# Optimization experiments

Hardware: AMD Instinct MI355X
Metric: run time of the kernel (lower is better)

Reference implementation:

```python
import jax, jax.numpy as jnp
import numpy as np

N, E = 50000, 800000
F_IN, HID, HEADS = 128, 32, 8
H1 = HID * HEADS            # 256: conv1 concat output, also conv2 in/out
NUM_WALKS, WALK_LEN = 512, 64
WINDOW, NEG_S = 5, 10
TEMP = 0.07
NEG_SLOPE = 0.2


def setup_inputs() -> dict:
    key = jax.random.key(0)
    ks = jax.random.split(key, 16)
    inp = {
        "x": jax.random.normal(ks[0], (N, F_IN), jnp.float32),
        "edge_index": jax.random.randint(ks[1], (2, E), 0, N),
        "walks": jax.random.randint(ks[2], (NUM_WALKS, WALK_LEN), 0, N),
        "neg_nodes": jax.random.randint(ks[3], (NUM_WALKS, WALK_LEN, NEG_S), 0, N),
        # conv1 params (GATConv: in=F_IN, out=HID, heads=HEADS, concat)
        "W1": jax.random.normal(ks[4], (F_IN, HEADS * HID), jnp.float32) / np.sqrt(F_IN),
        "a_src1": jax.random.normal(ks[5], (HEADS, HID), jnp.float32) / np.sqrt(HID),
        "a_dst1": jax.random.normal(ks[6], (HEADS, HID), jnp.float32) / np.sqrt(HID),
        "b1": jnp.zeros((HEADS * HID,), jnp.float32),
        # conv2 params (GATConv: in=H1, out=H1, heads=1)
        "W2": jax.random.normal(ks[7], (H1, H1), jnp.float32) / np.sqrt(H1),
        "a_src2": jax.random.normal(ks[8], (1, H1), jnp.float32) / np.sqrt(H1),
        "a_dst2": jax.random.normal(ks[9], (1, H1), jnp.float32) / np.sqrt(H1),
        "b2": jnp.zeros((H1,), jnp.float32),
    }
    return inp


def gat_conv(x, edge_index, W, a_src, a_dst, b, heads, out_ch):
    """PyG-style GATConv: self-loops, per-dst softmax attention, concat heads."""
    n = x.shape[0]
    loops = jnp.arange(n)
    src = jnp.concatenate([edge_index[0], loops])
    dst = jnp.concatenate([edge_index[1], loops])
    xw = (x @ W).reshape(n, heads, out_ch)                  # [N,H,C]
    al_s = jnp.einsum('nhc,hc->nh', xw, a_src)              # [N,H]
    al_d = jnp.einsum('nhc,hc->nh', xw, a_dst)
    e = jax.nn.leaky_relu(al_s[src] + al_d[dst], NEG_SLOPE)  # [Et,H]
    m = jax.ops.segment_max(e, dst, num_segments=n)
    ex = jnp.exp(e - m[dst])
    den = jax.ops.segment_sum(ex, dst, num_segments=n)
    alpha = ex / den[dst]                                    # [Et,H]
    out = jax.ops.segment_sum(alpha[:, :, None] * xw[src], dst, num_segments=n)
    return out.reshape(n, heads * out_ch) + b


def walk_contrastive_loss(emb, walks, neg_nodes):
    eps = 1e-8
    nrm = emb / jnp.clip(jnp.linalg.norm(emb, axis=-1, keepdims=True), eps)
    L = walks.shape[1]
    offs = jnp.concatenate([jnp.arange(-WINDOW, 0), jnp.arange(1, WINDOW + 1)])  # [2W]
    pos_pos = jnp.arange(L)[:, None] + offs[None, :]        # [L,2W]
    pos_valid = (pos_pos >= 0) & (pos_pos < L)
    pos_nodes = walks[:, jnp.clip(pos_pos, 0, L - 1)]       # [B,L,2W]
    anchor = nrm[walks]                                      # [B,L,D]
    pos_sims = jnp.einsum('bld,blpd->blp', anchor, nrm[pos_nodes]) / TEMP
    neg_sims = jnp.einsum('bld,blsd->bls', anchor, nrm[neg_nodes]) / TEMP
    # drop negatives that collide with (valid) positives, as torch.isin filter does
    neg_in_pos = ((neg_nodes[:, :, :, None] == pos_nodes[:, :, None, :])
                  & pos_valid[None, :, None, :]).any(-1)     # [B,L,S]
    pos_sum = jnp.sum(jnp.exp(pos_sims) * pos_valid[None].astype(emb.dtype), axis=-1)
    neg_sum = jnp.sum(jnp.exp(neg_sims) * (~neg_in_pos).astype(emb.dtype), axis=-1)
    has_pos = pos_valid.any(-1)[None]                        # [1,L]
    safe_pos = jnp.where(has_pos, pos_sum, 1.0)
    term = -jnp.log(safe_pos / (safe_pos + neg_sum))
    return jnp.sum(jnp.where(has_pos, term, 0.0))


def reference(x, edge_index, walks, neg_nodes, W1, a_src1, a_dst1, b1,
              W2, a_src2, a_dst2, b2):
    emb1 = jax.nn.elu(gat_conv(x, edge_index, W1, a_src1, a_dst1, b1, HEADS, HID))
    emb2 = gat_conv(emb1, edge_index, W2, a_src2, a_dst2, b2, 1, H1)
    emb = jnp.concatenate([emb1, emb2], axis=1)              # [N, 2*H1]
    return walk_contrastive_loss(emb, walks, neg_nodes)
```

## Files before the change

kernel.cpp:

```cpp
#include <hip/hip_runtime.h>
#include <math.h>

#define N_NODES 50000
#define N_PAD 50048
#define E_EDGES 800000
#define E_PAD (E_EDGES + 8 * N_NODES)
#define FDIM_IN 128
#define HID_1 32
#define HEADS_1 8
#define H1DIM 256
#define NUM_WALKS 512
#define WALK_LEN 64
#define WINDOW 5
#define NEG_S 10
#define TEMP 0.07f
#define INV_TEMP (1.0f / 0.07f)
#define NEG_SLOPE 0.2f
#define LOG2E 1.44269504f

#define SCAN_BLOCKS ((N_NODES + 255) / 256)

#define NB 98
#define NGRP 8
#define GCAP 1536
#define LCAP 32
#define BIN_BLOCKS 784

typedef unsigned int uint;
typedef unsigned short ushort;
typedef long long i64_t;
typedef __attribute__((ext_vector_type(8))) short bf16x8;
typedef __attribute__((ext_vector_type(8))) ushort us8;
typedef __attribute__((ext_vector_type(4))) float f32x4;
typedef __attribute__((ext_vector_type(2))) float vf2;
typedef __attribute__((ext_vector_type(2))) i64_t i64x2;
typedef __attribute__((ext_vector_type(4))) uint u32x4;

__device__ __forceinline__ float leaky(float v) {
    return fmaxf(v, v * NEG_SLOPE);
}

__device__ __forceinline__ float bfl(uint u) { return __uint_as_float(u << 16); }
__device__ __forceinline__ float bfh(uint u) { return __uint_as_float(u & 0xffff0000u); }

__device__ __forceinline__ ushort f2bf(float x) {
    uint u = __float_as_uint(x);
    u = u + 0x7fffu + ((u >> 16) & 1u);
    return (ushort)(u >> 16);
}

__device__ __forceinline__ uint pk4fp8(float a, float b, float c, float d) {
    int u = __builtin_amdgcn_cvt_pk_fp8_f32(a, b, 0, false);
    u = __builtin_amdgcn_cvt_pk_fp8_f32(c, d, u, true);
    return (uint)u;
}

__device__ __forceinline__ float red16(float x) {
    int v = __float_as_int(x);
    x += __int_as_float(__builtin_amdgcn_update_dpp(0, v, 0xB1, 0xF, 0xF, true));
    v = __float_as_int(x);
    x += __int_as_float(__builtin_amdgcn_update_dpp(0, v, 0x4E, 0xF, 0xF, true));
    v = __float_as_int(x);
    x += __int_as_float(__builtin_amdgcn_update_dpp(0, v, 0x141, 0xF, 0xF, true));
    v = __float_as_int(x);
    x += __int_as_float(__builtin_amdgcn_update_dpp(0, v, 0x140, 0xF, 0xF, true));
    return x;
}


#define PB_CVT  6250
#define PO_WT1  (PB_CVT)
#define PO_WT2  (PO_WT1 + 128)
#define PO_MISC (PO_WT2 + 256)
#define PO_BIN  (PO_MISC + 1)
#define PREP_GRID (PO_BIN + BIN_BLOCKS)

__global__ __launch_bounds__(256) void prep_kernel(
        const float* __restrict__ x, const int* __restrict__ ei,
        const float* __restrict__ W1, const float* __restrict__ W2,
        uint* __restrict__ xb, ushort* __restrict__ wt1, ushort* __restrict__ wt2,
        int* __restrict__ degp, uint* __restrict__ gbucket, int* __restrict__ gcur,
        float* __restrict__ als1, float* __restrict__ als2, uint* __restrict__ xw8) {
    const int blk = blockIdx.x, t = threadIdx.x;
    if (blk < PB_CVT) {
        int i = blk * 256 + t;
        float4 v = ((const float4*)x)[i];
        uint2 p;
        p.x = (uint)f2bf(v.x) | ((uint)f2bf(v.y) << 16);
        p.y = (uint)f2bf(v.z) | ((uint)f2bf(v.w) << 16);
        ((uint2*)xb)[i] = p;
    } else if (blk < PO_WT2) {
        int tid = (blk - PO_WT1) * 256 + t;
        int k = tid >> 8, n = tid & 255;
        wt1[n * 128 + k] = f2bf(W1[k * 256 + n]);
    } else if (blk < PO_MISC) {
        int tid = (blk - PO_WT2) * 256 + t;
        int k = tid >> 8, n = tid & 255;
        wt2[n * 256 + k] = f2bf(W2[k * 256 + n]);
    } else if (blk < PO_BIN) {
        if (t < HEADS_1) als1[N_NODES * HEADS_1 + t] = -1e30f;
        if (t == HEADS_1) als2[N_NODES] = -1e30f;
        if (t >= 64 && t < 128) xw8[N_NODES * 64 + (t - 64)] = 0u;
    } else {
        __shared__ int scnt[NB];
        __shared__ int gposs[NB];
        __shared__ uint sbuf[NB * LCAP];
        const int g = blk & 7;
        int* dg = degp + g * N_NODES;
        int* gc = gcur + g * NB;
        uint* gb = gbucket + (size_t)g * NB * GCAP;
        if (t < NB) scnt[t] = 0;
        __syncthreads();
        const int e0 = (blk - PO_BIN) * 1024;
#pragma unroll
        for (int k = 0; k < 4; k++) {
            int e = e0 + k * 256 + t;
            if (e < E_EDGES) {
                int dst = ei[E_EDGES + e];
                int src = ei[e];
                atomicAdd(&dg[dst], 1);
                uint packed = ((uint)dst << 16) | (uint)src;
                int bk = dst >> 9;
                int pos = atomicAdd(&scnt[bk], 1);
                if (pos < LCAP) sbuf[bk * LCAP + pos] = packed;
                else {
                    int gp = atomicAdd(&gc[bk], 1);
                    gb[bk * GCAP + gp] = packed;
                }
            }
        }
        __syncthreads();
        if (t < NB) {
            int c = scnt[t]; if (c > LCAP) c = LCAP;
            gposs[t] = atomicAdd(&gc[t], c);
            scnt[t] = c;
        }
        __syncthreads();
        const int w2 = t >> 6, lane = t & 63;
        for (int b2 = w2; b2 < NB; b2 += 4) {
            int c = scnt[b2], gp = gposs[b2];
            for (int i = lane; i < c; i += 64)
                gb[b2 * GCAP + gp + i] = sbuf[b2 * LCAP + i];
        }
    }
}


__global__ __launch_bounds__(256) void scan_a(const int* __restrict__ degp,
                                              int* __restrict__ excl,
                                              int* __restrict__ bsum) {
    __shared__ int s[256];
    int t = threadIdx.x;
    int i = blockIdx.x * 256 + t;
    int d = 0;
    if (i < N_NODES) {
#pragma unroll
        for (int g = 0; g < NGRP; g++) d += degp[g * N_NODES + i];
    }
    int v = (d + 7) & ~7;
    s[t] = v;
    __syncthreads();
    for (int off = 1; off < 256; off <<= 1) {
        int tmp = (t >= off) ? s[t - off] : 0;
        __syncthreads();
        s[t] += tmp;
        __syncthreads();
    }
    if (i < N_NODES) excl[i] = s[t] - v;
    if (t == 255) bsum[blockIdx.x] = s[255];
}

__global__ __launch_bounds__(256) void scan_b(int* __restrict__ bsum) {
    __shared__ int s[256];
    int t = threadIdx.x;
    int v = (t < SCAN_BLOCKS) ? bsum[t] : 0;
    s[t] = v;
    __syncthreads();
    for (int off = 1; off < 256; off <<= 1) {
        int tmp = (t >= off) ? s[t - off] : 0;
        __syncthreads();
        s[t] += tmp;
        __syncthreads();
    }
    if (t < SCAN_BLOCKS) bsum[t] = s[t] - v;
}

__global__ void scan_c2(const int* __restrict__ degp,
                        int* __restrict__ excl, const int* __restrict__ bsum,
                        int* __restrict__ row_start) {
    int i = blockIdx.x * blockDim.x + threadIdx.x;
    if (i < N_NODES) {
        int rs = excl[i] + bsum[i >> 8];
        row_start[i] = rs;
        if (i == N_NODES - 1) {
            int d = 0;
#pragma unroll
            for (int g = 0; g < NGRP; g++) d += degp[g * N_NODES + i];
            row_start[N_NODES] = rs + ((d + 7) & ~7);
        }
    }
}

template<int K, int H>
__global__ __launch_bounds__(256) void mfma_gemm64(
        const ushort* __restrict__ A,
        const ushort* __restrict__ Wt,
        uint* __restrict__ Y8,
        const float* __restrict__ a_src,
        const float* __restrict__ a_dst,
        float* __restrict__ als, float* __restrict__ ald,
        const uint* __restrict__ gbucket, const int* __restrict__ gcur,
        const int* __restrict__ row_start, ushort* __restrict__ srclist) {
    constexpr int KP = K + 8;
    constexpr int K8 = K / 8;
    constexpr int AS_BYTES = 64 * KP * 2;
    constexpr int SMEM_BYTES = (H == 8) ? 34816 : (AS_BYTES + 2560);
    __shared__ __align__(16) char smem[SMEM_BYTES];
    int m0;
    if (H == 8) {
        if (blockIdx.x < NB) {
            ushort* win = (ushort*)smem;
            int* cur = (int*)(smem + 32768);
            const int b = blockIdx.x, t = threadIdx.x;
            const int nlo = b << 9;
            const int nhi = (nlo + 512 < N_NODES) ? (nlo + 512) : N_NODES;
            const int base = row_start[nlo];
            const int end = row_start[nhi];
            const int span = end - base;
            for (int i = t; i < nhi - nlo; i += 256) cur[i] = row_start[nlo + i] - base;
            for (int i = t; i < span / 2; i += 256) ((uint*)win)[i] = 0xC350C350u;
            __syncthreads();
            for (int g = 0; g < NGRP; g++) {
                const uint* gb = gbucket + ((size_t)g * NB + b) * GCAP;
                const int cnt = gcur[g * NB + b];
                for (int i = t; i < cnt; i += 256) {
                    uint packed = gb[i];
                    int dst = packed >> 16;
                    int slot = atomicAdd(&cur[dst - nlo], 1);
                    win[slot] = (ushort)(packed & 0xffffu);
                }
            }
            __syncthreads();
            u32x4* d4 = (u32x4*)(srclist + base);
            const u32x4* s4 = (const u32x4*)win;
            for (int i = t; i < span / 8; i += 256) d4[i] = s4[i];
            return;
        }
        m0 = (blockIdx.x - NB) * 64;
    } else {
        m0 = blockIdx.x * 64;
    }
    ushort* As = (ushort*)smem;
    float (*sals)[5] = (float(*)[5])(smem + AS_BYTES);
    float (*sald)[5] = (float(*)[5])(smem + AS_BYTES + 1280);
    const int t = threadIdx.x;
    const uint4* Ag = (const uint4*)(A + (size_t)m0 * K);
    uint4* As4 = (uint4*)As;
    for (int i = t; i < 64 * K8; i += 256) {
        int r = i / K8, c8 = i % K8;
        As4[r * (K8 + 1) + c8] = Ag[i];
    }
    __syncthreads();
    const int wv = __builtin_amdgcn_readfirstlane(t >> 6);
    const int lane = t & 63;
    const int n0 = wv * 64;
    const int mrow = lane & 15, q = lane >> 4;
    f32x4 acc[4][4];
#pragma unroll
    for (int mt = 0; mt < 4; mt++)
#pragma unroll
        for (int i = 0; i < 4; i++) acc[mt][i] = (f32x4){0.f, 0.f, 0.f, 0.f};
#pragma unroll
    for (int k0 = 0; k0 < K; k0 += 32) {
        bf16x8 a[4], b[4];
#pragma unroll
        for (int mt = 0; mt < 4; mt++)
            a[mt] = *(const bf16x8*)(As + (mt * 16 + mrow) * KP + k0 + q * 8);
#pragma unroll
        for (int i = 0; i < 4; i++)
            b[i] = *(const bf16x8*)(Wt + (uint)(n0 + i * 16 + mrow) * K + k0 + q * 8);
#pragma unroll
        for (int mt = 0; mt < 4; mt++)
#pragma unroll
            for (int i = 0; i < 4; i++)
                acc[mt][i] = __builtin_amdgcn_mfma_f32_16x16x32_bf16(a[mt], b[i], acc[mt][i], 0, 0, 0);
    }
    {
        float as[4], ad[4];
#pragma unroll
        for (int i = 0; i < 4; i++) {
            as[i] = a_src[n0 + i * 16 + mrow];
            ad[i] = a_dst[n0 + i * 16 + mrow];
        }
#pragma unroll
        for (int mt = 0; mt < 4; mt++) {
#pragma unroll
            for (int r = 0; r < 4; r++) {
                const int row = m0 + mt * 16 + q * 4 + r;
                if (H == 8) {
                    float ps0 = acc[mt][0][r] * as[0] + acc[mt][1][r] * as[1];
                    float ps1 = acc[mt][2][r] * as[2] + acc[mt][3][r] * as[3];
                    float pd0 = acc[mt][0][r] * ad[0] + acc[mt][1][r] * ad[1];
                    float pd1 = acc[mt][2][r] * ad[2] + acc[mt][3][r] * ad[3];
#pragma unroll
                    for (int o = 1; o < 16; o <<= 1) {
                        ps0 += __shfl_xor(ps0, o, 64); ps1 += __shfl_xor(ps1, o, 64);
                        pd0 += __shfl_xor(pd0, o, 64); pd1 += __shfl_xor(pd1, o, 64);
                    }
                    if (mrow == 0 && row < N_NODES) {
                        als[row * 8 + 2 * wv] = ps0 * LOG2E;
                        als[row * 8 + 2 * wv + 1] = ps1 * LOG2E;
                        ald[row * 8 + 2 * wv] = pd0 * LOG2E;
                        ald[row * 8 + 2 * wv + 1] = pd1 * LOG2E;
                    }
                } else {
                    float ps = acc[mt][0][r] * as[0] + acc[mt][1][r] * as[1]
                             + acc[mt][2][r] * as[2] + acc[mt][3][r] * as[3];
                    float pd = acc[mt][0][r] * ad[0] + acc[mt][1][r] * ad[1]
                             + acc[mt][2][r] * ad[2] + acc[mt][3][r] * ad[3];
#pragma unroll
                    for (int o = 1; o < 16; o <<= 1) {
                        ps += __shfl_xor(ps, o, 64); pd += __shfl_xor(pd, o, 64);
                    }
                    if (mrow == 0) {
                        sals[mt * 16 + q * 4 + r][wv] = ps;
                        sald[mt * 16 + q * 4 + r][wv] = pd;
                    }
                }
            }
        }
    }
    __syncthreads();
    if (H == 1 && t < 64) {
        const int row = m0 + t;
        if (row < N_NODES) {
            als[row] = (sals[t][0] + sals[t][1] + sals[t][2] + sals[t][3]) * LOG2E;
            ald[row] = (sald[t][0] + sald[t][1] + sald[t][2] + sald[t][3]) * LOG2E;
        }
    }
    float* S = (float*)smem + wv * 16 * 68;
    const int prow = lane >> 2, pj = lane & 3;
#pragma unroll
    for (int mt = 0; mt < 4; mt++) {
#pragma unroll
        for (int i = 0; i < 4; i++)
#pragma unroll
            for (int r = 0; r < 4; r++)
                S[(q * 4 + r) * 68 + i * 16 + mrow] = acc[mt][i][r];
        const float* cp = S + prow * 68 + pj * 16;
        uint4 o;
        o.x = pk4fp8(cp[0],  cp[1],  cp[2],  cp[3]);
        o.y = pk4fp8(cp[4],  cp[5],  cp[6],  cp[7]);
        o.z = pk4fp8(cp[8],  cp[9],  cp[10], cp[11]);
        o.w = pk4fp8(cp[12], cp[13], cp[14], cp[15]);
        const int row = m0 + mt * 16 + prow;
        if (row < N_NODES)
            ((uint4*)(Y8 + (size_t)row * 64))[wv * 4 + pj] = o;
    }
}

__global__ __launch_bounds__(256) void gat_gather1(
        const int* __restrict__ row_start, const ushort* __restrict__ srclist,
        const float* __restrict__ als, const float* __restrict__ ald,
        const uint* __restrict__ xw8,
        const float* __restrict__ bias,
        ushort* __restrict__ emb1b) {
    const int wid = __builtin_amdgcn_readfirstlane(blockIdx.x * 4 + (threadIdx.x >> 6));
    const uint lane = threadIdx.x & 63;
    const uint h = lane >> 3;
    const float ald_n = ald[wid * HEADS_1 + h];
    const int beg = row_start[wid], end = row_start[wid + 1];

    float ex0 = __builtin_amdgcn_exp2f(leaky(als[wid * HEADS_1 + h] + ald_n));
    uint u = xw8[((uint)wid << 6) + lane];
    vf2 lo = __builtin_amdgcn_cvt_pk_f32_fp8((int)u, false);
    vf2 hi = __builtin_amdgcn_cvt_pk_f32_fp8((int)u, true);
    float den = ex0;
    vf2 exv0 = {ex0, ex0};
    vf2 a01 = exv0 * lo, a23 = exv0 * hi;

    for (int i = beg; i < end; i += 8) {
        us8 sv = *(const us8*)(srclist + i);
        uint rr[8]; float ee[8];
#pragma unroll
        for (int j = 0; j < 8; j++) rr[j] = xw8[((uint)sv[j] << 6) + lane];
#pragma unroll
        for (int j = 0; j < 8; j++) ee[j] = als[(uint)sv[j] * HEADS_1 + h];
#pragma unroll
        for (int j = 0; j < 8; j++) {
            float ex = __builtin_amdgcn_exp2f(leaky(ee[j] + ald_n));
            vf2 l2 = __builtin_amdgcn_cvt_pk_f32_fp8((int)rr[j], false);
            vf2 h2 = __builtin_amdgcn_cvt_pk_f32_fp8((int)rr[j], true);
            den += ex;
            vf2 exv = {ex, ex};
            a01 += exv * l2;
            a23 += exv * h2;
        }
    }
    float inv = 1.f / den;
    float4 bv = ((const float4*)bias)[lane];
    float4 r;
    r.x = a01[0] * inv + bv.x; r.y = a01[1] * inv + bv.y;
    r.z = a23[0] * inv + bv.z; r.w = a23[1] * inv + bv.w;
    r.x = r.x > 0.f ? r.x : __expf(r.x) - 1.f;
    r.y = r.y > 0.f ? r.y : __expf(r.y) - 1.f;
    r.z = r.z > 0.f ? r.z : __expf(r.z) - 1.f;
    r.w = r.w > 0.f ? r.w : __expf(r.w) - 1.f;
    uint2 p;
    p.x = (uint)f2bf(r.x) | ((uint)f2bf(r.y) << 16);
    p.y = (uint)f2bf(r.z) | ((uint)f2bf(r.w) << 16);
    ((uint2*)emb1b)[((uint)wid << 6) + lane] = p;
}

__global__ __launch_bounds__(256) void gat_gather2(
        const int* __restrict__ row_start, const ushort* __restrict__ srclist,
        const float* __restrict__ als, const float* __restrict__ ald,
        const uint* __restrict__ xw8,
        const float* __restrict__ bias,
        const ushort* __restrict__ emb1b,
        uint* __restrict__ embn8) {
    const int wid = __builtin_amdgcn_readfirstlane(blockIdx.x * 4 + (threadIdx.x >> 6));
    const uint lane = threadIdx.x & 63;
    const float ald_n = ald[wid];
    const int beg = row_start[wid], end = row_start[wid + 1];

    float ex0 = __builtin_amdgcn_exp2f(leaky(als[wid] + ald_n));
    uint u = xw8[((uint)wid << 6) + lane];
    vf2 lo = __builtin_amdgcn_cvt_pk_f32_fp8((int)u, false);
    vf2 hi = __builtin_amdgcn_cvt_pk_f32_fp8((int)u, true);
    float den = ex0;
    vf2 exv0 = {ex0, ex0};
    vf2 a01 = exv0 * lo, a23 = exv0 * hi;

    for (int i = beg; i < end; i += 8) {
        us8 sv = *(const us8*)(srclist + i);
        uint rr[8]; float ee[8];
#pragma unroll
        for (int j = 0; j < 8; j++) rr[j] = xw8[((uint)sv[j] << 6) + lane];
#pragma unroll
        for (int j = 0; j < 8; j++) ee[j] = als[(uint)sv[j]];
#pragma unroll
        for (int j = 0; j < 8; j++) {
            float ex = __builtin_amdgcn_exp2f(leaky(ee[j] + ald_n));
            vf2 l2 = __builtin_amdgcn_cvt_pk_f32_fp8((int)rr[j], false);
            vf2 h2 = __builtin_amdgcn_cvt_pk_f32_fp8((int)rr[j], true);
            den += ex;
            vf2 exv = {ex, ex};
            a01 += exv * l2;
            a23 += exv * h2;
        }
    }
    float inv = 1.f / den;
    float4 bv = ((const float4*)bias)[lane];
    float4 e2;
    e2.x = a01[0] * inv + bv.x; e2.y = a01[1] * inv + bv.y;
    e2.z = a23[0] * inv + bv.z; e2.w = a23[1] * inv + bv.w;
    uint2 u1 = ((const uint2*)emb1b)[((uint)wid << 6) + lane];
    float4 e1;
    e1.x = bfl(u1.x); e1.y = bfh(u1.x); e1.z = bfl(u1.y); e1.w = bfh(u1.y);

    float ssum = e1.x * e1.x + e1.y * e1.y + e1.z * e1.z + e1.w * e1.w
               + e2.x * e2.x + e2.y * e2.y + e2.z * e2.z + e2.w * e2.w;
#pragma unroll
    for (int o = 32; o > 0; o >>= 1) ssum += __shfl_xor(ssum, o, 64);
    float innv = 1.f / fmaxf(sqrtf(ssum), 1e-8f);

    uint p1 = pk4fp8(e1.x * innv, e1.y * innv, e1.z * innv, e1.w * innv);
    uint p2 = pk4fp8(e2.x * innv, e2.y * innv, e2.z * innv, e2.w * innv);
    const uint n1 = ((lane >> 4) << 4) | (((lane >> 1) & 3) << 2) | (((lane >> 3) & 1) << 1) | (lane & 1);
    embn8[((uint)wid << 7) + n1] = p1;
    embn8[((uint)wid << 7) + 64 + n1] = p2;
}


#define ROWU 140

__global__ __launch_bounds__(1024, 8) void loss_mfma_kernel(
        const uint* __restrict__ embn8,
        const int* __restrict__ walks, const int* __restrict__ negs,
        float* __restrict__ out) {
    __shared__ __align__(16) uint srows8[WALK_LEN * ROWU];
    __shared__ int wids[WALK_LEN];
    __shared__ float possum[WALK_LEN];
    __shared__ float negsum[WALK_LEN];
    const int b = blockIdx.x;
    const int t = threadIdx.x;
    const int w = __builtin_amdgcn_readfirstlane(t >> 6);
    const int lane = t & 63;
    const int mrow = lane & 15, q = lane >> 4;
    const char* embc = (const char*)embn8;

    if (t < 64) wids[t] = walks[b * WALK_LEN + t];
    else if (t < 128) possum[t - 64] = 0.f;
    else if (t < 192) negsum[t - 128] = 0.f;

    uint4 Bv[8];
    int pnode = negs[b * (WALK_LEN * NEG_S) + (w * 16 + mrow)];
    {
        const char* bp = embc + (((uint)pnode) << 9) + (uint)(q * 16);
#pragma unroll
        for (int j = 0; j < 8; j++) Bv[j] = *(const uint4*)(bp + j * 64);
    }
    __syncthreads();

    {
        const int rA = w * 4 + (lane >> 5);
        const int rB = rA + 2;
        const uint off = lane & 31;
        ((uint4*)(srows8 + rA * ROWU))[off] = ((const uint4*)embn8)[((uint)wids[rA] << 5) + off];
        ((uint4*)(srows8 + rB * ROWU))[off] = ((const uint4*)embn8)[((uint)wids[rB] << 5) + off];
    }
    __syncthreads();

#pragma unroll
    for (int ji = 0; ji < 3; ji++) {
        const int job = w + ji * 16;
        f32x4 acc0 = {0.f, 0.f, 0.f, 0.f};
        f32x4 acc1 = {0.f, 0.f, 0.f, 0.f};
        if (ji < 2 || w < 8) {
            const int albase = (job / 10) * 16;
            const int curnode = pnode;
            const int owner = (job * 16 + mrow) / 10;
            const char* ap = (const char*)(srows8 + (albase + mrow) * ROWU) + q * 16;
            __builtin_amdgcn_s_setprio(1);
#pragma unroll
            for (int j = 0; j < 4; j++) {
                i64x2 a = *(const i64x2*)(ap + j * 64);
                const i64x2 bb = *(const i64x2*)&Bv[j];
                acc0 = __builtin_amdgcn_mfma_f32_16x16x32_fp8_fp8(a[0], bb[0], acc0, 0, 0, 0);
                acc0 = __builtin_amdgcn_mfma_f32_16x16x32_fp8_fp8(a[1], bb[1], acc0, 0, 0, 0);
            }
#pragma unroll
            for (int j = 4; j < 8; j++) {
                i64x2 a = *(const i64x2*)(ap + j * 64);
                const i64x2 bb = *(const i64x2*)&Bv[j];
                acc1 = __builtin_amdgcn_mfma_f32_16x16x32_fp8_fp8(a[0], bb[0], acc1, 0, 0, 0);
                acc1 = __builtin_amdgcn_mfma_f32_16x16x32_fp8_fp8(a[1], bb[1], acc1, 0, 0, 0);
            }
            __builtin_amdgcn_s_setprio(0);
            if (ji == 0 || (ji == 1 && w < 8)) {
                const int njob = job + 16;
                pnode = negs[b * (WALK_LEN * NEG_S) + (njob * 16 + mrow)];
                const char* bp = embc + (((uint)pnode) << 9) + (uint)(q * 16);
#pragma unroll
                for (int j = 0; j < 8; j++) Bv[j] = *(const uint4*)(bp + j * 64);
            }
#pragma unroll
            for (int reg = 0; reg < 4; reg++) {
                const int l_a = albase + q * 4 + reg;
                float e = 0.f;
                if (owner == l_a) {
                    bool msk = false;
#pragma unroll
                    for (int dj = -WINDOW; dj <= WINDOW; dj++) {
                        if (dj == 0) continue;
                        int p = l_a + dj;
                        if (p >= 0 && p < WALK_LEN && wids[p] == curnode) msk = true;
                    }
                    if (!msk) e = __expf((acc0[reg] + acc1[reg]) * INV_TEMP);
                }
                e = red16(e);
                if (mrow == 0 && e != 0.f) atomicAdd(&negsum[l_a], e);
            }
        } else {
            const int pj = w - 8;
            const int g = pj >> 1, half = pj & 1;
            const int albase = g * 16;
            const int base = (albase - WINDOW) > 0 ? (albase - WINDOW) : 0;
            const int hi = (albase + 15 + WINDOW) < (WALK_LEN - 1) ? (albase + 15 + WINDOW) : (WALK_LEN - 1);
            const int cnt = hi - base + 1;
            const int r = half * 16 + mrow;
            const int row = base + r;
            const int rc = row < hi ? row : hi;
            const char* ap = (const char*)(srows8 + (albase + mrow) * ROWU) + q * 16;
            const char* bp = (const char*)(srows8 + rc * ROWU) + q * 16;
            __builtin_amdgcn_s_setprio(1);
#pragma unroll
            for (int j = 0; j < 4; j++) {
                i64x2 a = *(const i64x2*)(ap + j * 64);
                i64x2 bb = *(const i64x2*)(bp + j * 64);
                acc0 = __builtin_amdgcn_mfma_f32_16x16x32_fp8_fp8(a[0], bb[0], acc0, 0, 0, 0);
                acc0 = __builtin_amdgcn_mfma_f32_16x16x32_fp8_fp8(a[1], bb[1], acc0, 0, 0, 0);
            }
#pragma unroll
            for (int j = 4; j < 8; j++) {
                i64x2 a = *(const i64x2*)(ap + j * 64);
                i64x2 bb = *(const i64x2*)(bp + j * 64);
                acc1 = __builtin_amdgcn_mfma_f32_16x16x32_fp8_fp8(a[0], bb[0], acc1, 0, 0, 0);
                acc1 = __builtin_amdgcn_mfma_f32_16x16x32_fp8_fp8(a[1], bb[1], acc1, 0, 0, 0);
            }
            __builtin_amdgcn_s_setprio(0);
#pragma unroll
            for (int reg = 0; reg < 4; reg++) {
                const int l_a = albase + q * 4 + reg;
                const int d = row - l_a;
                bool use = (r < cnt) && (d != 0) && (d >= -WINDOW) && (d <= WINDOW);
                float e = use ? __expf((acc0[reg] + acc1[reg]) * INV_TEMP) : 0.f;
                e = red16(e);
                if (mrow == 0 && e != 0.f) atomicAdd(&possum[l_a], e);
            }
        }
    }
    __syncthreads();
    if (t < 64) {
        float term = logf(1.f + negsum[t] / possum[t]);
#pragma unroll
        for (int o = 32; o > 0; o >>= 1) term += __shfl_xor(term, o, 64);
        if (t == 0) atomicAdd(out, term);
    }
}

extern "C" void kernel_launch(void* const* d_in, const int* in_sizes, int n_in,
                              void* d_out, int out_size, void* d_ws, size_t ws_size,
                              hipStream_t stream) {
    const float* x      = (const float*)d_in[0];
    const int*   ei     = (const int*)d_in[1];
    const int*   walks  = (const int*)d_in[2];
    const int*   negs   = (const int*)d_in[3];
    const float* W1     = (const float*)d_in[4];
    const float* a_src1 = (const float*)d_in[5];
    const float* a_dst1 = (const float*)d_in[6];
    const float* b1     = (const float*)d_in[7];
    const float* W2     = (const float*)d_in[8];
    const float* a_src2 = (const float*)d_in[9];
    const float* a_dst2 = (const float*)d_in[10];
    const float* b2     = (const float*)d_in[11];
    float* out = (float*)d_out;

    float* ws = (float*)d_ws;
    size_t off = 0;
#define ALIGN_OFF off = (off + 255) & ~(size_t)255
    float* r_xw8   = ws + off; off += (size_t)(N_NODES + 1) * 64;  ALIGN_OFF;
    float* r_emb1b = ws + off; off += (size_t)N_PAD * 128;         ALIGN_OFF;
    float* r_embn8 = ws + off; off += (size_t)N_NODES * 128;       ALIGN_OFF;
    float* r_xb    = ws + off; off += (size_t)N_PAD * 64;          ALIGN_OFF;
    float* r_wt1   = ws + off; off += 256 * 64;                    ALIGN_OFF;
    float* r_wt2   = ws + off; off += 256 * 128;                   ALIGN_OFF;
    float* als1  = ws + off; off += (N_NODES + 1) * HEADS_1;       ALIGN_OFF;
    float* ald1  = ws + off; off += N_NODES * HEADS_1;             ALIGN_OFF;
    float* als2  = ws + off; off += N_NODES + 1;                   ALIGN_OFF;
    float* ald2  = ws + off; off += N_NODES;                       ALIGN_OFF;
    int* degp      = (int*)(ws + off); off += (size_t)NGRP * N_NODES; ALIGN_OFF;
    int* excl      = (int*)(ws + off); off += N_NODES;             ALIGN_OFF;
    int* bsum      = (int*)(ws + off); off += 256;                 ALIGN_OFF;
    int* row_start = (int*)(ws + off); off += N_NODES + 1;         ALIGN_OFF;
    uint* gbucket  = (uint*)(ws + off); off += (size_t)NGRP * NB * GCAP; ALIGN_OFF;
    int* gcur      = (int*)(ws + off); off += 1024;                ALIGN_OFF;
    ushort* srclist = (ushort*)(ws + off); off += E_PAD / 2;       ALIGN_OFF;
    uint*   xw8   = (uint*)r_xw8;
    ushort* emb1b = (ushort*)r_emb1b;
    uint*   embn8 = (uint*)r_embn8;
    ushort* xb    = (ushort*)r_xb;
    ushort* wt1   = (ushort*)r_wt1;
    ushort* wt2   = (ushort*)r_wt2;

    hipMemsetAsync(out, 0, sizeof(float) * out_size, stream);
    hipMemsetAsync(degp, 0, sizeof(int) * NGRP * N_NODES, stream);
    hipMemsetAsync(gcur, 0, sizeof(int) * NGRP * NB, stream);

    prep_kernel<<<PREP_GRID, 256, 0, stream>>>(
        x, ei, W1, W2, (uint*)xb, wt1, wt2, degp, gbucket, gcur, als1, als2, xw8);

    scan_a<<<SCAN_BLOCKS, 256, 0, stream>>>(degp, excl, bsum);
    scan_b<<<1, 256, 0, stream>>>(bsum);
    scan_c2<<<SCAN_BLOCKS, 256, 0, stream>>>(degp, excl, bsum, row_start);

    mfma_gemm64<128, HEADS_1><<<NB + N_PAD / 64, 256, 0, stream>>>(
        xb, wt1, xw8, a_src1, a_dst1, als1, ald1, gbucket, gcur, row_start, srclist);
    gat_gather1<<<N_NODES / 4, 256, 0, stream>>>(
        row_start, srclist, als1, ald1, xw8, b1, emb1b);

    mfma_gemm64<256, 1><<<N_PAD / 64, 256, 0, stream>>>(
        emb1b, wt2, xw8, a_src2, a_dst2, als2, ald2, gbucket, gcur, row_start, srclist);
    gat_gather2<<<N_NODES / 4, 256, 0, stream>>>(
        row_start, srclist, als2, ald2, xw8, b2, emb1b, embn8);

    loss_mfma_kernel<<<NUM_WALKS, 1024, 0, stream>>>(embn8, walks, negs, out);
}
```

Measured before the change: 316.6 us.

## Derive node degrees from destination buckets instead of global atomic counters

Drops the global per-node atomic degree histogram (and its memset) from the edge binning pass. The scan now counts degrees per 512-node bucket with shared-memory atomics over the already-binned edges, and scans two nodes per thread. The block-sum scan is resized to the 98 buckets and writes the final row_start entry. This removes 800K global atomics and a 1.6MB memset, at the cost of a second read of the bucket arrays in the scan.

```diff
diff --git a/kernel.cpp b/kernel.cpp
--- a/kernel.cpp
+++ b/kernel.cpp
@@ -79,7 +79,7 @@
         const float* __restrict__ x, const int* __restrict__ ei,
         const float* __restrict__ W1, const float* __restrict__ W2,
         uint* __restrict__ xb, ushort* __restrict__ wt1, ushort* __restrict__ wt2,
-        int* __restrict__ degp, uint* __restrict__ gbucket, int* __restrict__ gcur,
+        uint* __restrict__ gbucket, int* __restrict__ gcur,
         float* __restrict__ als1, float* __restrict__ als2, uint* __restrict__ xw8) {
     const int blk = blockIdx.x, t = threadIdx.x;
     if (blk < PB_CVT) {
@@ -106,7 +106,6 @@
         __shared__ int gposs[NB];
         __shared__ uint sbuf[NB * LCAP];
         const int g = blk & 7;
-        int* dg = degp + g * N_NODES;
         int* gc = gcur + g * NB;
         uint* gb = gbucket + (size_t)g * NB * GCAP;
         if (t < NB) scnt[t] = 0;
@@ -118,7 +117,6 @@
             if (e < E_EDGES) {
                 int dst = ei[E_EDGES + e];
                 int src = ei[e];
-                atomicAdd(&dg[dst], 1);
                 uint packed = ((uint)dst << 16) | (uint)src;
                 int bk = dst >> 9;
                 int pos = atomicAdd(&scnt[bk], 1);
@@ -146,19 +144,26 @@
 }
 
 
-__global__ __launch_bounds__(256) void scan_a(const int* __restrict__ degp,
-                                              int* __restrict__ excl,
-                                              int* __restrict__ bsum) {
+__global__ __launch_bounds__(256) void scan_a(
+        const uint* __restrict__ gbucket, const int* __restrict__ gcur,
+        int* __restrict__ excl, int* __restrict__ bsum) {
+    __shared__ int cnt[512];
     __shared__ int s[256];
-    int t = threadIdx.x;
-    int i = blockIdx.x * 256 + t;
-    int d = 0;
-    if (i < N_NODES) {
-#pragma unroll
-        for (int g = 0; g < NGRP; g++) d += degp[g * N_NODES + i];
-    }
-    int v = (d + 7) & ~7;
-    s[t] = v;
+    const int b = blockIdx.x, t = threadIdx.x;
+    const int nlo = b << 9;
+    cnt[t] = 0; cnt[t + 256] = 0;
+    __syncthreads();
+    for (int g = 0; g < NGRP; g++) {
+        const uint* gb = gbucket + ((size_t)g * NB + b) * GCAP;
+        const int c = gcur[g * NB + b];
+        for (int i = t; i < c; i += 256)
+            atomicAdd(&cnt[(gb[i] >> 16) - nlo], 1);
+    }
+    __syncthreads();
+    const int v0 = (cnt[2 * t] + 7) & ~7;
+    const int v1 = (cnt[2 * t + 1] + 7) & ~7;
+    const int vs = v0 + v1;
+    s[t] = vs;
     __syncthreads();
     for (int off = 1; off < 256; off <<= 1) {
         int tmp = (t >= off) ? s[t - off] : 0;
@@ -166,39 +171,33 @@
         s[t] += tmp;
         __syncthreads();
     }
-    if (i < N_NODES) excl[i] = s[t] - v;
-    if (t == 255) bsum[blockIdx.x] = s[255];
-}
-
-__global__ __launch_bounds__(256) void scan_b(int* __restrict__ bsum) {
-    __shared__ int s[256];
+    const int ex = s[t] - vs;
+    const int n0 = nlo + 2 * t;
+    if (n0 < N_NODES) excl[n0] = ex;
+    if (n0 + 1 < N_NODES) excl[n0 + 1] = ex + v0;
+    if (t == 255) bsum[b] = s[255];
+}
+
+__global__ __launch_bounds__(128) void scan_b(int* __restrict__ bsum, int* __restrict__ row_start) {
+    __shared__ int s[128];
     int t = threadIdx.x;
-    int v = (t < SCAN_BLOCKS) ? bsum[t] : 0;
+    int v = (t < NB) ? bsum[t] : 0;
     s[t] = v;
     __syncthreads();
-    for (int off = 1; off < 256; off <<= 1) {
+    for (int off = 1; off < 128; off <<= 1) {
         int tmp = (t >= off) ? s[t - off] : 0;
         __syncthreads();
         s[t] += tmp;
         __syncthreads();
     }
-    if (t < SCAN_BLOCKS) bsum[t] = s[t] - v;
-}
-
-__global__ void scan_c2(const int* __restrict__ degp,
-                        int* __restrict__ excl, const int* __restrict__ bsum,
+    if (t < NB) bsum[t] = s[t] - v;
+    if (t == 127) row_start[N_NODES] = s[127];
+}
+
+__global__ void scan_c2(const int* __restrict__ excl, const int* __restrict__ bsum,
                         int* __restrict__ row_start) {
     int i = blockIdx.x * blockDim.x + threadIdx.x;
-    if (i < N_NODES) {
-        int rs = excl[i] + bsum[i >> 8];
-        row_start[i] = rs;
-        if (i == N_NODES - 1) {
-            int d = 0;
-#pragma unroll
-            for (int g = 0; g < NGRP; g++) d += degp[g * N_NODES + i];
-            row_start[N_NODES] = rs + ((d + 7) & ~7);
-        }
-    }
+    if (i < N_NODES) row_start[i] = excl[i] + bsum[i >> 9];
 }
 
 template<int K, int H>
@@ -640,7 +639,6 @@
     float* ald1  = ws + off; off += N_NODES * HEADS_1;             ALIGN_OFF;
     float* als2  = ws + off; off += N_NODES + 1;                   ALIGN_OFF;
     float* ald2  = ws + off; off += N_NODES;                       ALIGN_OFF;
-    int* degp      = (int*)(ws + off); off += (size_t)NGRP * N_NODES; ALIGN_OFF;
     int* excl      = (int*)(ws + off); off += N_NODES;             ALIGN_OFF;
     int* bsum      = (int*)(ws + off); off += 256;                 ALIGN_OFF;
     int* row_start = (int*)(ws + off); off += N_NODES + 1;         ALIGN_OFF;
@@ -655,15 +653,14 @@
     ushort* wt2   = (ushort*)r_wt2;
 
     hipMemsetAsync(out, 0, sizeof(float) * out_size, stream);
-    hipMemsetAsync(degp, 0, sizeof(int) * NGRP * N_NODES, stream);
     hipMemsetAsync(gcur, 0, sizeof(int) * NGRP * NB, stream);
 
     prep_kernel<<<PREP_GRID, 256, 0, stream>>>(
-        x, ei, W1, W2, (uint*)xb, wt1, wt2, degp, gbucket, gcur, als1, als2, xw8);
-
-    scan_a<<<SCAN_BLOCKS, 256, 0, stream>>>(degp, excl, bsum);
-    scan_b<<<1, 256, 0, stream>>>(bsum);
-    scan_c2<<<SCAN_BLOCKS, 256, 0, stream>>>(degp, excl, bsum, row_start);
+        x, ei, W1, W2, (uint*)xb, wt1, wt2, gbucket, gcur, als1, als2, xw8);
+
+    scan_a<<<NB, 256, 0, stream>>>(gbucket, gcur, excl, bsum);
+    scan_b<<<1, 128, 0, stream>>>(bsum, row_start);
+    scan_c2<<<SCAN_BLOCKS, 256, 0, stream>>>(excl, bsum, row_start);
 
     mfma_gemm64<128, HEADS_1><<<NB + N_PAD / 64, 256, 0, stream>>>(
         xb, wt1, xw8, a_src1, a_dst1, als1, ald1, gbucket, gcur, row_start, srclist);
```

After: 292.6 us. 7.6% less time.
